# Performance work log

Measured on AMD Instinct MI355X. Metric: run time of the kernel, lower is better.

## Reference

```python
import jax, jax.numpy as jnp
import numpy as np


def _seg_mean(feat, idx, n):
    # mean aggregation with zero-degree clamp (PyG mean aggr semantics)
    s = jax.ops.segment_sum(feat, idx, num_segments=n)
    c = jax.ops.segment_sum(jnp.ones((idx.shape[0],), feat.dtype), idx, num_segments=n)
    return s / jnp.maximum(c, 1.0)[:, None]


def setup_inputs() -> dict:
    key = jax.random.key(0)
    ks = jax.random.split(key, 10)
    Nu, Nr, D, H, E = 200000, 50000, 64, 64, 2000000
    scale = 1.0 / np.sqrt(D)
    return {
        "x_user": jax.random.normal(ks[0], (Nu, D), jnp.float32),
        "x_res": jax.random.normal(ks[1], (Nr, D), jnp.float32),
        "src_u": jax.random.randint(ks[2], (E,), 0, Nu, jnp.int64 if jax.config.jax_enable_x64 else jnp.int32),
        "dst_r": jax.random.randint(ks[3], (E,), 0, Nr, jnp.int64 if jax.config.jax_enable_x64 else jnp.int32),
        "Wl_ur": jax.random.normal(ks[4], (D, H), jnp.float32) * scale,
        "bl_ur": jnp.zeros((H,), jnp.float32),
        "Wr_ur": jax.random.normal(ks[5], (D, H), jnp.float32) * scale,
        "Wl_ru": jax.random.normal(ks[6], (D, H), jnp.float32) * scale,
        "bl_ru": jnp.zeros((H,), jnp.float32),
        "Wr_ru": jax.random.normal(ks[7], (D, H), jnp.float32) * scale,
    }


def reference(x_user, x_res, src_u, dst_r, Wl_ur, bl_ur, Wr_ur, Wl_ru, bl_ru, Wr_ru):
    Nu, Nr = x_user.shape[0], x_res.shape[0]
    # relation ('user','accessed','resource'): gather user feats along edges, mean-scatter to resources
    agg_r = _seg_mean(x_user[src_u], dst_r, Nr)              # [Nr, D]
    out_res = agg_r @ Wl_ur + bl_ur + x_res @ Wr_ur           # SAGEConv: lin_l(aggr) + lin_r(root)
    # relation ('resource','rev_accessed','user'): reversed edges
    agg_u = _seg_mean(x_res[dst_r], src_u, Nu)               # [Nu, D]
    out_user = agg_u @ Wl_ru + bl_ru + x_user @ Wr_ru
    # relu (+ dropout as identity in eval mode)
    return (jax.nn.relu(out_res), jax.nn.relu(out_user))
```

## Files before the change

### kernel.cpp

```cpp
#include <hip/hip_runtime.h>


__global__ void count_pers_kernel(const int* __restrict__ src, const int* __restrict__ dst,
                                  int* __restrict__ cnt, int Nr, int nE,
                                  float invR, float invU, int nq)
{
    const int p  = blockIdx.x & 7;
    const int q  = blockIdx.x >> 3;
    const int e0 = (int)((long long)q * nE / nq);
    const int e1 = (int)((long long)(q + 1) * nE / nq);
    for (int e = e0 + threadIdx.x; e < e1; e += blockDim.x) {
        const int dr = dst[e];
        const int su = src[e];
        if (min(7, (int)(dr * invR)) == p) atomicAdd(&cnt[dr], 1);
        if (min(7, (int)(su * invU)) == p) atomicAdd(&cnt[Nr + su], 1);
    }
}

#define SCAN_BS 2048

__global__ void scan_block_kernel(const int* __restrict__ cnt, int* __restrict__ off,
                                  int* __restrict__ partial, int N)
{
    __shared__ int sdata[256];
    const int t = threadIdx.x;
    const long long base = (long long)blockIdx.x * SCAN_BS + (long long)t * 8;
    int v[8];
    int s = 0;
    #pragma unroll
    for (int k = 0; k < 8; ++k) {
        long long i = base + k;
        v[k] = (i < N) ? cnt[i] : 0;
        s += v[k];
    }
    sdata[t] = s;
    __syncthreads();
    for (int d = 1; d < 256; d <<= 1) {
        int val = (t >= d) ? sdata[t - d] : 0;
        __syncthreads();
        if (t >= d) sdata[t] += val;
        __syncthreads();
    }
    if (t == 255) partial[blockIdx.x] = sdata[255];
    int run = sdata[t] - s;
    #pragma unroll
    for (int k = 0; k < 8; ++k) {
        long long i = base + k;
        if (i < N) off[i] = run;
        run += v[k];
    }
}

__global__ void scan_partials_kernel(int* __restrict__ partial, int nb)
{
    __shared__ int sdata[256];
    const int t = threadIdx.x;
    int v = (t < nb) ? partial[t] : 0;
    sdata[t] = v;
    __syncthreads();
    for (int d = 1; d < 256; d <<= 1) {
        int val = (t >= d) ? sdata[t - d] : 0;
        __syncthreads();
        if (t >= d) sdata[t] += val;
        __syncthreads();
    }
    if (t < nb) partial[t] = sdata[t] - v;
}

__global__ void scan_addback_kernel(int* __restrict__ off, const int* __restrict__ partial,
                                    int N, int total)
{
    long long i = (long long)blockIdx.x * blockDim.x + threadIdx.x;
    if (i < N) off[i] += partial[i / SCAN_BS];
    if (i == 0) off[N] = total;
}

__global__ void scatter_pers_kernel(const int* __restrict__ src, const int* __restrict__ dst,
                                    const int* __restrict__ off, int* __restrict__ cnt,
                                    int* __restrict__ nbr, int Nr, int nE,
                                    float invR, float invU, int nq)
{
    const int p  = blockIdx.x & 7;
    const int q  = blockIdx.x >> 3;
    const int e0 = (int)((long long)q * nE / nq);
    const int e1 = (int)((long long)(q + 1) * nE / nq);
    for (int e = e0 + threadIdx.x; e < e1; e += blockDim.x) {
        const int dr = dst[e];
        const int su = src[e];
        if (min(7, (int)(dr * invR)) == p) {
            int pos = off[dr] + atomicSub(&cnt[dr], 1) - 1;
            nbr[pos] = su;
        }
        if (min(7, (int)(su * invU)) == p) {
            int pos = off[Nr + su] + atomicSub(&cnt[Nr + su], 1) - 1;
            nbr[pos] = dr;
        }
    }
}

__device__ __forceinline__ unsigned short f2bf(float f) {
    unsigned u = __float_as_uint(f);
    return (unsigned short)((u + 0x7FFF + ((u >> 16) & 1)) >> 16);
}

__global__ void tobf16_kernel(const float* __restrict__ x, unsigned short* __restrict__ y,
                              long long n4)
{
    long long i = (long long)blockIdx.x * blockDim.x + threadIdx.x;
    if (i >= n4) return;
    const float4 v = reinterpret_cast<const float4*>(x)[i];
    ushort4 o;
    o.x = f2bf(v.x); o.y = f2bf(v.y); o.z = f2bf(v.z); o.w = f2bf(v.w);
    reinterpret_cast<ushort4*>(y)[i] = o;
}

__device__ __forceinline__ float bf2f(unsigned short h) {
    return __uint_as_float((unsigned)h << 16);
}

__device__ __forceinline__ void bfadd(float4& a, const ushort4 v) {
    a.x += bf2f(v.x); a.y += bf2f(v.y); a.z += bf2f(v.z); a.w += bf2f(v.w);
}

__global__ void gather_bf16_kernel(const unsigned short* __restrict__ xub,
                                   const unsigned short* __restrict__ xrb,
                                   const int* __restrict__ off,
                                   const int* __restrict__ nbr,
                                   float* __restrict__ out, int Nr, int NN)
{
    const int tid  = blockIdx.x * blockDim.x + threadIdx.x;
    const int g    = tid >> 4;
    if (g >= NN) return;
    const int lane = tid & 15;
    const int c    = lane << 2;
    const unsigned short* __restrict__ x = (g < Nr) ? xub : xrb;

    const int beg = off[g];
    const int end = off[g + 1];

    float4 a0 = {0,0,0,0}, a1 = {0,0,0,0}, a2 = {0,0,0,0}, a3 = {0,0,0,0};
    int j = beg;
    for (; j + 4 <= end; j += 4) {
        const int s0 = nbr[j], s1 = nbr[j+1], s2 = nbr[j+2], s3 = nbr[j+3];
        bfadd(a0, *reinterpret_cast<const ushort4*>(x + ((long long)s0 << 6) + c));
        bfadd(a1, *reinterpret_cast<const ushort4*>(x + ((long long)s1 << 6) + c));
        bfadd(a2, *reinterpret_cast<const ushort4*>(x + ((long long)s2 << 6) + c));
        bfadd(a3, *reinterpret_cast<const ushort4*>(x + ((long long)s3 << 6) + c));
    }
    for (; j < end; ++j) {
        bfadd(a0, *reinterpret_cast<const ushort4*>(x + ((long long)nbr[j] << 6) + c));
    }
    a0.x += a1.x + a2.x + a3.x;
    a0.y += a1.y + a2.y + a3.y;
    a0.z += a1.z + a2.z + a3.z;
    a0.w += a1.w + a2.w + a3.w;

    const float inv = 1.0f / (float)max(end - beg, 1);
    float4 r; r.x = a0.x * inv; r.y = a0.y * inv; r.z = a0.z * inv; r.w = a0.w * inv;
    *reinterpret_cast<float4*>(out + ((long long)g << 6) + c) = r;
}

__device__ __forceinline__ void f4add(float4& a, const float4 v) {
    a.x += v.x; a.y += v.y; a.z += v.z; a.w += v.w;
}

__global__ void gather_mean_all_kernel(const float* __restrict__ xu,
                                       const float* __restrict__ xr,
                                       const int* __restrict__ off,
                                       const int* __restrict__ nbr,
                                       float* __restrict__ out, int Nr, int NN)
{
    const int tid  = blockIdx.x * blockDim.x + threadIdx.x;
    const int g    = tid >> 4;
    if (g >= NN) return;
    const int lane = tid & 15;
    const int c    = lane << 2;
    const float* __restrict__ x = (g < Nr) ? xu : xr;

    const int beg = off[g];
    const int end = off[g + 1];

    float4 a0 = {0,0,0,0}, a1 = {0,0,0,0}, a2 = {0,0,0,0}, a3 = {0,0,0,0};
    int j = beg;
    for (; j + 4 <= end; j += 4) {
        const int s0 = nbr[j], s1 = nbr[j+1], s2 = nbr[j+2], s3 = nbr[j+3];
        f4add(a0, *reinterpret_cast<const float4*>(x + ((long long)s0 << 6) + c));
        f4add(a1, *reinterpret_cast<const float4*>(x + ((long long)s1 << 6) + c));
        f4add(a2, *reinterpret_cast<const float4*>(x + ((long long)s2 << 6) + c));
        f4add(a3, *reinterpret_cast<const float4*>(x + ((long long)s3 << 6) + c));
    }
    for (; j < end; ++j) {
        f4add(a0, *reinterpret_cast<const float4*>(x + ((long long)nbr[j] << 6) + c));
    }
    f4add(a0, a1); f4add(a2, a3); f4add(a0, a2);

    const float inv = 1.0f / (float)max(end - beg, 1);
    float4 r; r.x = a0.x * inv; r.y = a0.y * inv; r.z = a0.z * inv; r.w = a0.w * inv;
    *reinterpret_cast<float4*>(out + ((long long)g << 6) + c) = r;
}

__device__ __forceinline__ float rlane(float v, int l) {
    return __int_as_float(__builtin_amdgcn_readlane(__float_as_int(v), l));
}

#define LWV(nm, W, i) \
    float4 nm; nm.x = W[(4*(i)+0)*64 + lane]; nm.y = W[(4*(i)+1)*64 + lane]; \
    nm.z = W[(4*(i)+2)*64 + lane]; nm.w = W[(4*(i)+3)*64 + lane];

#define TSTEP(i, acc) { \
    acc = fmaf(rlane(va, 4*(i)+0), wl##i.x, acc); \
    acc = fmaf(rlane(va, 4*(i)+1), wl##i.y, acc); \
    acc = fmaf(rlane(va, 4*(i)+2), wl##i.z, acc); \
    acc = fmaf(rlane(va, 4*(i)+3), wl##i.w, acc); \
    acc = fmaf(rlane(vx, 4*(i)+0), wr##i.x, acc); \
    acc = fmaf(rlane(vx, 4*(i)+1), wr##i.y, acc); \
    acc = fmaf(rlane(vx, 4*(i)+2), wr##i.z, acc); \
    acc = fmaf(rlane(vx, 4*(i)+3), wr##i.w, acc); }

__global__ __launch_bounds__(256, 3)
void transform_v4_kernel(const float* __restrict__ agg,
                         const float* __restrict__ xroot,
                         const float* __restrict__ Wl,
                         const float* __restrict__ bl,
                         const float* __restrict__ Wr,
                         float* __restrict__ out, int N)
{
    const int lane = threadIdx.x & 63;
    const int wid  = (blockIdx.x * blockDim.x + threadIdx.x) >> 6;
    const int nw   = (gridDim.x * blockDim.x) >> 6;

    LWV(wl0,  Wl, 0)  LWV(wl1,  Wl, 1)  LWV(wl2,  Wl, 2)  LWV(wl3,  Wl, 3)
    LWV(wl4,  Wl, 4)  LWV(wl5,  Wl, 5)  LWV(wl6,  Wl, 6)  LWV(wl7,  Wl, 7)
    LWV(wl8,  Wl, 8)  LWV(wl9,  Wl, 9)  LWV(wl10, Wl, 10) LWV(wl11, Wl, 11)
    LWV(wl12, Wl, 12) LWV(wl13, Wl, 13) LWV(wl14, Wl, 14) LWV(wl15, Wl, 15)
    LWV(wr0,  Wr, 0)  LWV(wr1,  Wr, 1)  LWV(wr2,  Wr, 2)  LWV(wr3,  Wr, 3)
    LWV(wr4,  Wr, 4)  LWV(wr5,  Wr, 5)  LWV(wr6,  Wr, 6)  LWV(wr7,  Wr, 7)
    LWV(wr8,  Wr, 8)  LWV(wr9,  Wr, 9)  LWV(wr10, Wr, 10) LWV(wr11, Wr, 11)
    LWV(wr12, Wr, 12) LWV(wr13, Wr, 13) LWV(wr14, Wr, 14) LWV(wr15, Wr, 15)
    const float bias = bl[lane];

    for (int r = wid; r < N; r += nw) {
        const long long base = (long long)r << 6;
        const float va = agg[base + lane];
        const float vx = xroot[base + lane];
        float acc0 = bias, acc1 = 0.f, acc2 = 0.f, acc3 = 0.f;
        TSTEP(0,  acc0) TSTEP(1,  acc1) TSTEP(2,  acc2) TSTEP(3,  acc3)
        TSTEP(4,  acc0) TSTEP(5,  acc1) TSTEP(6,  acc2) TSTEP(7,  acc3)
        TSTEP(8,  acc0) TSTEP(9,  acc1) TSTEP(10, acc2) TSTEP(11, acc3)
        TSTEP(12, acc0) TSTEP(13, acc1) TSTEP(14, acc2) TSTEP(15, acc3)
        const float acc = (acc0 + acc1) + (acc2 + acc3);
        out[base + lane] = fmaxf(acc, 0.0f);
    }
}

__global__ void edge_scatter_kernel(
    const float* __restrict__ xu, const float* __restrict__ xr,
    const int* __restrict__ src, const int* __restrict__ dst,
    float* __restrict__ agg_r, float* __restrict__ agg_u,
    float* __restrict__ deg_r, float* __restrict__ deg_u,
    int nE)
{
    int tid  = blockIdx.x * blockDim.x + threadIdx.x;
    int e    = tid >> 4;
    if (e >= nE) return;
    int lane = tid & 15;
    int su = src[e];
    int dr = dst[e];
    if (lane == 0) {
        atomicAdd(&deg_r[dr], 1.0f);
        atomicAdd(&deg_u[su], 1.0f);
    }
    const float4 a = *reinterpret_cast<const float4*>(xu + ((long long)su << 6) + (lane << 2));
    const float4 b = *reinterpret_cast<const float4*>(xr + ((long long)dr << 6) + (lane << 2));
    float* pr = agg_r + ((long long)dr << 6) + (lane << 2);
    float* pu = agg_u + ((long long)su << 6) + (lane << 2);
    atomicAdd(pr + 0, a.x); atomicAdd(pr + 1, a.y);
    atomicAdd(pr + 2, a.z); atomicAdd(pr + 3, a.w);
    atomicAdd(pu + 0, b.x); atomicAdd(pu + 1, b.y);
    atomicAdd(pu + 2, b.z); atomicAdd(pu + 3, b.w);
}

__global__ void transform_kernel(
    const float* __restrict__ agg, const float* __restrict__ deg,
    const float* __restrict__ xroot,
    const float* __restrict__ Wl, const float* __restrict__ bl,
    const float* __restrict__ Wr,
    float* __restrict__ out, int N)
{
    __shared__ float sWl[64 * 64];
    __shared__ float sWr[64 * 64];
    __shared__ float sb[64];
    __shared__ float sAgg[4][64];
    __shared__ float sX[4][64];

    const int t = threadIdx.x;
    for (int i = t; i < 64 * 64; i += 256) {
        sWl[i] = Wl[i];
        sWr[i] = Wr[i];
    }
    if (t < 64) sb[t] = bl[t];
    __syncthreads();

    const int rg = t >> 6;
    const int h  = t & 63;

    for (long long r0 = (long long)blockIdx.x * 4; r0 < N; r0 += (long long)gridDim.x * 4) {
        const long long r = r0 + rg;
        if (r < N) {
            float inv = 1.0f / fmaxf(deg[r], 1.0f);
            sAgg[rg][h] = agg[(r << 6) + h] * inv;
            sX[rg][h]   = xroot[(r << 6) + h];
        }
        __syncthreads();
        if (r < N) {
            float acc = sb[h];
            #pragma unroll
            for (int d = 0; d < 64; ++d) {
                acc += sAgg[rg][d] * sWl[d * 64 + h] + sX[rg][d] * sWr[d * 64 + h];
            }
            out[(r << 6) + h] = fmaxf(acc, 0.0f);
        }
        __syncthreads();
    }
}

extern "C" void kernel_launch(void* const* d_in, const int* in_sizes, int n_in,
                              void* d_out, int out_size, void* d_ws, size_t ws_size,
                              hipStream_t stream)
{
    const float* xu    = (const float*)d_in[0];
    const float* xr    = (const float*)d_in[1];
    const int*   src   = (const int*)  d_in[2];
    const int*   dst   = (const int*)  d_in[3];
    const float* Wl_ur = (const float*)d_in[4];
    const float* bl_ur = (const float*)d_in[5];
    const float* Wr_ur = (const float*)d_in[6];
    const float* Wl_ru = (const float*)d_in[7];
    const float* bl_ru = (const float*)d_in[8];
    const float* Wr_ru = (const float*)d_in[9];

    const int Nu = in_sizes[0] / 64;
    const int Nr = in_sizes[1] / 64;
    const int nE = in_sizes[2];
    const int NN = Nr + Nu;

    float* out   = (float*)d_out;
    float* agg_r = out;
    float* agg_u = out + (long long)Nr * 64;

    int* cnt     = (int*)d_ws;
    int* off     = cnt + NN;
    int* partial = off + NN + 1;
    int* nbr     = partial + 256;
    uintptr_t bfBase = ((uintptr_t)(nbr + 2ull * nE) + 15) & ~(uintptr_t)15;
    unsigned short* xub = (unsigned short*)bfBase;
    unsigned short* xrb = xub + (size_t)Nu * 64;
    const size_t needCsr = ((size_t)NN + NN + 1 + 256 + 2ull * nE) * sizeof(int);
    const size_t needBf  = (bfBase - (uintptr_t)d_ws) + (size_t)(Nu + Nr) * 64 * sizeof(unsigned short);

    if (ws_size >= needCsr) {
        hipMemsetAsync(cnt, 0, (size_t)NN * sizeof(int), stream);

        const bool useBf = (ws_size >= needBf);
        if (useBf) {
            const long long n4u = (long long)Nu * 16;
            const long long n4r = (long long)Nr * 16;
            tobf16_kernel<<<(int)((n4u + 255) / 256), 256, 0, stream>>>(xu, xub, n4u);
            tobf16_kernel<<<(int)((n4r + 255) / 256), 256, 0, stream>>>(xr, xrb, n4r);
        }

        const float invR = 8.0f / (float)Nr;
        const float invU = 8.0f / (float)Nu;
        const int PG = 2048;
        const int nq = PG >> 3;

        count_pers_kernel<<<PG, 256, 0, stream>>>(src, dst, cnt, Nr, nE, invR, invU, nq);

        const int nScanBlocks = (NN + SCAN_BS - 1) / SCAN_BS;
        scan_block_kernel<<<nScanBlocks, 256, 0, stream>>>(cnt, off, partial, NN);
        scan_partials_kernel<<<1, 256, 0, stream>>>(partial, nScanBlocks);
        scan_addback_kernel<<<(NN + 255) / 256, 256, 0, stream>>>(off, partial, NN, 2 * nE);

        scatter_pers_kernel<<<PG, 256, 0, stream>>>(
            src, dst, off, cnt, nbr, Nr, nE, invR, invU, nq);

        {
            const long long tg = (long long)NN * 16;
            const int gblocks = (int)((tg + 255) / 256);
            if (useBf) {
                gather_bf16_kernel<<<gblocks, 256, 0, stream>>>(
                    xub, xrb, off, nbr, out, Nr, NN);
            } else {
                gather_mean_all_kernel<<<gblocks, 256, 0, stream>>>(
                    xu, xr, off, nbr, out, Nr, NN);
            }
        }

        transform_v4_kernel<<<1024, 256, 0, stream>>>(
            agg_r, xr, Wl_ur, bl_ur, Wr_ur, agg_r, Nr);
        transform_v4_kernel<<<1024, 256, 0, stream>>>(
            agg_u, xu, Wl_ru, bl_ru, Wr_ru, agg_u, Nu);
    } else {
        float* deg_r = (float*)d_ws;
        float* deg_u = deg_r + Nr;
        hipMemsetAsync(d_out, 0, (size_t)out_size * sizeof(float), stream);
        hipMemsetAsync(d_ws, 0, (size_t)NN * sizeof(float), stream);

        const long long total = (long long)nE * 16;
        edge_scatter_kernel<<<(int)((total + 255) / 256), 256, 0, stream>>>(
            xu, xr, src, dst, agg_r, agg_u, deg_r, deg_u, nE);

        transform_kernel<<<2048, 256, 0, stream>>>(
            agg_r, deg_r, xr, Wl_ur, bl_ur, Wr_ur, agg_r, Nr);
        transform_kernel<<<2048, 256, 0, stream>>>(
            agg_u, deg_u, xu, Wl_ru, bl_ru, Wr_ru, agg_u, Nu);
    }
}
```

Baseline: 700.4 us.

## Use bf16 MFMA for SAGE linear transforms and simplify degree counting

Replaces the readlane-based fp32 transform with a bf16 MFMA kernel (16x16x32) that reads bf16 aggregates and bf16 root features. It adds a weight-transpose/convert prep kernel, and makes the gather write bf16 aggregates to workspace. The partitioned count kernel is replaced by a plain one-pass atomic count. This trades precision (bf16 inputs to the GEMM) for fewer ALU cycles and less memory traffic, and it needs more workspace.

```diff
diff --git a/kernel.cpp b/kernel.cpp
--- a/kernel.cpp
+++ b/kernel.cpp
@@ -1,20 +1,16 @@
 #include <hip/hip_runtime.h>
 
 
-__global__ void count_pers_kernel(const int* __restrict__ src, const int* __restrict__ dst,
-                                  int* __restrict__ cnt, int Nr, int nE,
-                                  float invR, float invU, int nq)
-{
-    const int p  = blockIdx.x & 7;
-    const int q  = blockIdx.x >> 3;
-    const int e0 = (int)((long long)q * nE / nq);
-    const int e1 = (int)((long long)(q + 1) * nE / nq);
-    for (int e = e0 + threadIdx.x; e < e1; e += blockDim.x) {
-        const int dr = dst[e];
-        const int su = src[e];
-        if (min(7, (int)(dr * invR)) == p) atomicAdd(&cnt[dr], 1);
-        if (min(7, (int)(su * invU)) == p) atomicAdd(&cnt[Nr + su], 1);
-    }
+typedef __attribute__((ext_vector_type(8))) short bf16x8;
+typedef __attribute__((ext_vector_type(4))) float f32x4;
+
+__global__ void count_kernel(const int* __restrict__ src, const int* __restrict__ dst,
+                             int* __restrict__ cnt, int Nr, int nE)
+{
+    int e = blockIdx.x * blockDim.x + threadIdx.x;
+    if (e >= nE) return;
+    atomicAdd(&cnt[dst[e]], 1);
+    atomicAdd(&cnt[Nr + src[e]], 1);
 }
 
 #define SCAN_BS 2048
@@ -102,6 +98,9 @@
     unsigned u = __float_as_uint(f);
     return (unsigned short)((u + 0x7FFF + ((u >> 16) & 1)) >> 16);
 }
+__device__ __forceinline__ float bf2f(unsigned short h) {
+    return __uint_as_float((unsigned)h << 16);
+}
 
 __global__ void tobf16_kernel(const float* __restrict__ x, unsigned short* __restrict__ y,
                               long long n4)
@@ -114,19 +113,28 @@
     reinterpret_cast<ushort4*>(y)[i] = o;
 }
 
-__device__ __forceinline__ float bf2f(unsigned short h) {
-    return __uint_as_float((unsigned)h << 16);
+__global__ void wprep_kernel(const float* __restrict__ W0, const float* __restrict__ W1,
+                             const float* __restrict__ W2, const float* __restrict__ W3,
+                             unsigned short* __restrict__ Wt)
+{
+    int i = blockIdx.x * blockDim.x + threadIdx.x;
+    if (i >= 4 * 4096) return;
+    const int mat = i >> 12, r = i & 4095, col = r >> 6, k = r & 63;
+    const float* W = (mat == 0) ? W0 : (mat == 1) ? W1 : (mat == 2) ? W2 : W3;
+    Wt[i] = f2bf(W[k * 64 + col]);
 }
 
 __device__ __forceinline__ void bfadd(float4& a, const ushort4 v) {
     a.x += bf2f(v.x); a.y += bf2f(v.y); a.z += bf2f(v.z); a.w += bf2f(v.w);
 }
 
-__global__ void gather_bf16_kernel(const unsigned short* __restrict__ xub,
-                                   const unsigned short* __restrict__ xrb,
-                                   const int* __restrict__ off,
-                                   const int* __restrict__ nbr,
-                                   float* __restrict__ out, int Nr, int NN)
+template <bool BF_OUT>
+__device__ __forceinline__ void gather_body(const unsigned short* __restrict__ xub,
+                                            const unsigned short* __restrict__ xrb,
+                                            const int* __restrict__ off,
+                                            const int* __restrict__ nbr,
+                                            float* fout, unsigned short* bout,
+                                            int Nr, int NN)
 {
     const int tid  = blockIdx.x * blockDim.x + threadIdx.x;
     const int g    = tid >> 4;
@@ -156,9 +164,28 @@
     a0.w += a1.w + a2.w + a3.w;
 
     const float inv = 1.0f / (float)max(end - beg, 1);
-    float4 r; r.x = a0.x * inv; r.y = a0.y * inv; r.z = a0.z * inv; r.w = a0.w * inv;
-    *reinterpret_cast<float4*>(out + ((long long)g << 6) + c) = r;
-}
+    if (BF_OUT) {
+        ushort4 o;
+        o.x = f2bf(a0.x * inv); o.y = f2bf(a0.y * inv);
+        o.z = f2bf(a0.z * inv); o.w = f2bf(a0.w * inv);
+        *reinterpret_cast<ushort4*>(bout + ((long long)g << 6) + c) = o;
+    } else {
+        float4 r; r.x = a0.x * inv; r.y = a0.y * inv; r.z = a0.z * inv; r.w = a0.w * inv;
+        *reinterpret_cast<float4*>(fout + ((long long)g << 6) + c) = r;
+    }
+}
+
+__global__ void gather_bf16b_kernel(const unsigned short* __restrict__ xub,
+                                    const unsigned short* __restrict__ xrb,
+                                    const int* __restrict__ off, const int* __restrict__ nbr,
+                                    unsigned short* __restrict__ aggb, int Nr, int NN)
+{ gather_body<true>(xub, xrb, off, nbr, nullptr, aggb, Nr, NN); }
+
+__global__ void gather_bf16_kernel(const unsigned short* __restrict__ xub,
+                                   const unsigned short* __restrict__ xrb,
+                                   const int* __restrict__ off, const int* __restrict__ nbr,
+                                   float* __restrict__ out, int Nr, int NN)
+{ gather_body<false>(xub, xrb, off, nbr, out, nullptr, Nr, NN); }
 
 __device__ __forceinline__ void f4add(float4& a, const float4 v) {
     a.x += v.x; a.y += v.y; a.z += v.z; a.w += v.w;
@@ -176,10 +203,8 @@
     const int lane = tid & 15;
     const int c    = lane << 2;
     const float* __restrict__ x = (g < Nr) ? xu : xr;
-
     const int beg = off[g];
     const int end = off[g + 1];
-
     float4 a0 = {0,0,0,0}, a1 = {0,0,0,0}, a2 = {0,0,0,0}, a3 = {0,0,0,0};
     int j = beg;
     for (; j + 4 <= end; j += 4) {
@@ -189,14 +214,89 @@
         f4add(a2, *reinterpret_cast<const float4*>(x + ((long long)s2 << 6) + c));
         f4add(a3, *reinterpret_cast<const float4*>(x + ((long long)s3 << 6) + c));
     }
-    for (; j < end; ++j) {
+    for (; j < end; ++j)
         f4add(a0, *reinterpret_cast<const float4*>(x + ((long long)nbr[j] << 6) + c));
-    }
     f4add(a0, a1); f4add(a2, a3); f4add(a0, a2);
-
     const float inv = 1.0f / (float)max(end - beg, 1);
     float4 r; r.x = a0.x * inv; r.y = a0.y * inv; r.z = a0.z * inv; r.w = a0.w * inv;
     *reinterpret_cast<float4*>(out + ((long long)g << 6) + c) = r;
+}
+
+#define WFRAG(P, n, ks) (*reinterpret_cast<const bf16x8*>((P) + ((n)*16 + l15)*64 + (ks)*32 + l4*8))
+
+__global__ __launch_bounds__(256, 2)
+void transform_mfma_kernel(const unsigned short* __restrict__ aggb,
+                           const unsigned short* __restrict__ xb,
+                           const unsigned short* __restrict__ Wlt,
+                           const unsigned short* __restrict__ Wrt,
+                           const float* __restrict__ bl,
+                           float* __restrict__ out, int N)
+{
+    const int lane = threadIdx.x & 63;
+    const int l15  = lane & 15;
+    const int l4   = lane >> 4;
+    const int wid  = (blockIdx.x * blockDim.x + threadIdx.x) >> 6;
+    const int nTiles = (N + 15) >> 4;
+    if (wid >= nTiles) return;
+
+    const bf16x8 wl00 = WFRAG(Wlt, 0, 0), wl01 = WFRAG(Wlt, 0, 1);
+    const bf16x8 wl10 = WFRAG(Wlt, 1, 0), wl11 = WFRAG(Wlt, 1, 1);
+    const bf16x8 wl20 = WFRAG(Wlt, 2, 0), wl21 = WFRAG(Wlt, 2, 1);
+    const bf16x8 wl30 = WFRAG(Wlt, 3, 0), wl31 = WFRAG(Wlt, 3, 1);
+    const bf16x8 wr00 = WFRAG(Wrt, 0, 0), wr01 = WFRAG(Wrt, 0, 1);
+    const bf16x8 wr10 = WFRAG(Wrt, 1, 0), wr11 = WFRAG(Wrt, 1, 1);
+    const bf16x8 wr20 = WFRAG(Wrt, 2, 0), wr21 = WFRAG(Wrt, 2, 1);
+    const bf16x8 wr30 = WFRAG(Wrt, 3, 0), wr31 = WFRAG(Wrt, 3, 1);
+
+    const float b0 = bl[l15], b1 = bl[16 + l15], b2 = bl[32 + l15], b3 = bl[48 + l15];
+
+    const int tb = wid << 4;
+    const int arow = min(tb + l15, N - 1);
+    const unsigned short* pa = aggb + (long long)arow * 64;
+    const unsigned short* px = xb   + (long long)arow * 64;
+
+    const bf16x8 a0 = *reinterpret_cast<const bf16x8*>(pa + l4 * 8);
+    const bf16x8 a1 = *reinterpret_cast<const bf16x8*>(pa + 32 + l4 * 8);
+    const bf16x8 x0 = *reinterpret_cast<const bf16x8*>(px + l4 * 8);
+    const bf16x8 x1 = *reinterpret_cast<const bf16x8*>(px + 32 + l4 * 8);
+
+    f32x4 acc0 = {b0, b0, b0, b0};
+    f32x4 acc1 = {b1, b1, b1, b1};
+    f32x4 acc2 = {b2, b2, b2, b2};
+    f32x4 acc3 = {b3, b3, b3, b3};
+
+    acc0 = __builtin_amdgcn_mfma_f32_16x16x32_bf16(a0, wl00, acc0, 0, 0, 0);
+    acc0 = __builtin_amdgcn_mfma_f32_16x16x32_bf16(a1, wl01, acc0, 0, 0, 0);
+    acc0 = __builtin_amdgcn_mfma_f32_16x16x32_bf16(x0, wr00, acc0, 0, 0, 0);
+    acc0 = __builtin_amdgcn_mfma_f32_16x16x32_bf16(x1, wr01, acc0, 0, 0, 0);
+
+    acc1 = __builtin_amdgcn_mfma_f32_16x16x32_bf16(a0, wl10, acc1, 0, 0, 0);
+    acc1 = __builtin_amdgcn_mfma_f32_16x16x32_bf16(a1, wl11, acc1, 0, 0, 0);
+    acc1 = __builtin_amdgcn_mfma_f32_16x16x32_bf16(x0, wr10, acc1, 0, 0, 0);
+    acc1 = __builtin_amdgcn_mfma_f32_16x16x32_bf16(x1, wr11, acc1, 0, 0, 0);
+
+    acc2 = __builtin_amdgcn_mfma_f32_16x16x32_bf16(a0, wl20, acc2, 0, 0, 0);
+    acc2 = __builtin_amdgcn_mfma_f32_16x16x32_bf16(a1, wl21, acc2, 0, 0, 0);
+    acc2 = __builtin_amdgcn_mfma_f32_16x16x32_bf16(x0, wr20, acc2, 0, 0, 0);
+    acc2 = __builtin_amdgcn_mfma_f32_16x16x32_bf16(x1, wr21, acc2, 0, 0, 0);
+
+    acc3 = __builtin_amdgcn_mfma_f32_16x16x32_bf16(a0, wl30, acc3, 0, 0, 0);
+    acc3 = __builtin_amdgcn_mfma_f32_16x16x32_bf16(a1, wl31, acc3, 0, 0, 0);
+    acc3 = __builtin_amdgcn_mfma_f32_16x16x32_bf16(x0, wr30, acc3, 0, 0, 0);
+    acc3 = __builtin_amdgcn_mfma_f32_16x16x32_bf16(x1, wr31, acc3, 0, 0, 0);
+
+    float* po = out + (long long)tb * 64;
+    #pragma unroll
+    for (int r = 0; r < 4; ++r) {
+        const int row = tb + l4 * 4 + r;
+        if (row < N) {
+            float* prow = po + (long long)(l4 * 4 + r) * 64 + l15;
+            prow[0]  = fmaxf(acc0[r], 0.0f);
+            prow[16] = fmaxf(acc1[r], 0.0f);
+            prow[32] = fmaxf(acc2[r], 0.0f);
+            prow[48] = fmaxf(acc3[r], 0.0f);
+        }
+    }
 }
 
 __device__ __forceinline__ float rlane(float v, int l) {
@@ -353,53 +453,70 @@
     int* partial = off + NN + 1;
     int* nbr     = partial + 256;
     uintptr_t bfBase = ((uintptr_t)(nbr + 2ull * nE) + 15) & ~(uintptr_t)15;
-    unsigned short* xub = (unsigned short*)bfBase;
-    unsigned short* xrb = xub + (size_t)Nu * 64;
-    const size_t needCsr = ((size_t)NN + NN + 1 + 256 + 2ull * nE) * sizeof(int);
-    const size_t needBf  = (bfBase - (uintptr_t)d_ws) + (size_t)(Nu + Nr) * 64 * sizeof(unsigned short);
+    unsigned short* xub  = (unsigned short*)bfBase;
+    unsigned short* xrb  = xub + (size_t)Nu * 64;
+    unsigned short* aggb = xrb + (size_t)Nr * 64;
+    unsigned short* Wt   = aggb + (size_t)NN * 64;
+    const size_t needCsr  = ((size_t)NN + NN + 1 + 256 + 2ull * nE) * sizeof(int);
+    const size_t needBf   = (bfBase - (uintptr_t)d_ws) + (size_t)NN * 64 * 2;
+    const size_t needMfma = (bfBase - (uintptr_t)d_ws)
+                          + ((size_t)NN * 64 + (size_t)NN * 64 + 4 * 4096) * 2;
 
     if (ws_size >= needCsr) {
         hipMemsetAsync(cnt, 0, (size_t)NN * sizeof(int), stream);
 
-        const bool useBf = (ws_size >= needBf);
+        const bool useBf   = (ws_size >= needBf);
+        const bool useMfma = (ws_size >= needMfma);
         if (useBf) {
             const long long n4u = (long long)Nu * 16;
             const long long n4r = (long long)Nr * 16;
             tobf16_kernel<<<(int)((n4u + 255) / 256), 256, 0, stream>>>(xu, xub, n4u);
             tobf16_kernel<<<(int)((n4r + 255) / 256), 256, 0, stream>>>(xr, xrb, n4r);
         }
-
-        const float invR = 8.0f / (float)Nr;
-        const float invU = 8.0f / (float)Nu;
-        const int PG = 2048;
-        const int nq = PG >> 3;
-
-        count_pers_kernel<<<PG, 256, 0, stream>>>(src, dst, cnt, Nr, nE, invR, invU, nq);
+        if (useMfma) {
+            wprep_kernel<<<64, 256, 0, stream>>>(Wl_ur, Wr_ur, Wl_ru, Wr_ru, Wt);
+        }
+
+        count_kernel<<<(nE + 255) / 256, 256, 0, stream>>>(src, dst, cnt, Nr, nE);
 
         const int nScanBlocks = (NN + SCAN_BS - 1) / SCAN_BS;
         scan_block_kernel<<<nScanBlocks, 256, 0, stream>>>(cnt, off, partial, NN);
         scan_partials_kernel<<<1, 256, 0, stream>>>(partial, nScanBlocks);
         scan_addback_kernel<<<(NN + 255) / 256, 256, 0, stream>>>(off, partial, NN, 2 * nE);
 
+        const float invR = 8.0f / (float)Nr;
+        const float invU = 8.0f / (float)Nu;
+        const int PG = 2048;
         scatter_pers_kernel<<<PG, 256, 0, stream>>>(
-            src, dst, off, cnt, nbr, Nr, nE, invR, invU, nq);
-
-        {
-            const long long tg = (long long)NN * 16;
-            const int gblocks = (int)((tg + 255) / 256);
-            if (useBf) {
-                gather_bf16_kernel<<<gblocks, 256, 0, stream>>>(
-                    xub, xrb, off, nbr, out, Nr, NN);
-            } else {
-                gather_mean_all_kernel<<<gblocks, 256, 0, stream>>>(
-                    xu, xr, off, nbr, out, Nr, NN);
-            }
-        }
-
-        transform_v4_kernel<<<1024, 256, 0, stream>>>(
-            agg_r, xr, Wl_ur, bl_ur, Wr_ur, agg_r, Nr);
-        transform_v4_kernel<<<1024, 256, 0, stream>>>(
-            agg_u, xu, Wl_ru, bl_ru, Wr_ru, agg_u, Nu);
+            src, dst, off, cnt, nbr, Nr, nE, invR, invU, PG >> 3);
+
+        const long long tg = (long long)NN * 16;
+        const int gblocks = (int)((tg + 255) / 256);
+
+        if (useMfma) {
+            gather_bf16b_kernel<<<gblocks, 256, 0, stream>>>(
+                xub, xrb, off, nbr, aggb, Nr, NN);
+            const int tilesR = (Nr + 15) / 16;
+            const int tilesU = (Nu + 15) / 16;
+            transform_mfma_kernel<<<(tilesR + 3) / 4, 256, 0, stream>>>(
+                aggb, xrb, Wt, Wt + 4096, bl_ur, agg_r, Nr);
+            transform_mfma_kernel<<<(tilesU + 3) / 4, 256, 0, stream>>>(
+                aggb + (size_t)Nr * 64, xub, Wt + 2 * 4096, Wt + 3 * 4096, bl_ru, agg_u, Nu);
+        } else if (useBf) {
+            gather_bf16_kernel<<<gblocks, 256, 0, stream>>>(
+                xub, xrb, off, nbr, out, Nr, NN);
+            transform_v4_kernel<<<1024, 256, 0, stream>>>(
+                agg_r, xr, Wl_ur, bl_ur, Wr_ur, agg_r, Nr);
+            transform_v4_kernel<<<1024, 256, 0, stream>>>(
+                agg_u, xu, Wl_ru, bl_ru, Wr_ru, agg_u, Nu);
+        } else {
+            gather_mean_all_kernel<<<gblocks, 256, 0, stream>>>(
+                xu, xr, off, nbr, out, Nr, NN);
+            transform_v4_kernel<<<1024, 256, 0, stream>>>(
+                agg_r, xr, Wl_ur, bl_ur, Wr_ur, agg_r, Nr);
+            transform_v4_kernel<<<1024, 256, 0, stream>>>(
+                agg_u, xu, Wl_ru, bl_ru, Wr_ru, agg_u, Nu);
+        }
     } else {
         float* deg_r = (float*)d_ws;
         float* deg_u = deg_r + Nr;
```

Result: faster. 631.4 us (-9.9%).
